# Kernel tuning notes

Measured on AMD Instinct MI355X. Metric: run time of the kernel, lower is better.

The kernel has to match this reference:

```python
import jax, jax.numpy as jnp
import numpy as np

N = 100000   # nodes
E = 1600000  # edges
D = 64       # hidden_channels (heads=1, concat)
NEG_SLOPE = 0.2


def setup_inputs() -> dict:
    key = jax.random.key(0)
    ks = jax.random.split(key, 16)
    s = (1.0 / np.sqrt(D)).astype(np.float32) if hasattr(np.sqrt(D), 'astype') else 1.0 / np.sqrt(D)
    s = 1.0 / float(np.sqrt(D))
    inp = {
        "x": jax.random.normal(ks[0], (N, D), jnp.float32),
        "edge_index": jax.random.randint(ks[1], (2, E), 0, N, dtype=jnp.int32).astype(jnp.int64),
        "edge_attr": jax.random.normal(ks[2], (E, 1), jnp.float32),
        # layer 1 params (PyG GATConv, heads=1): lin, lin_edge, att_src, att_dst, att_edge, bias
        "W1":  jax.random.normal(ks[3], (D, D), jnp.float32) * s,
        "We1": jax.random.normal(ks[4], (1, D), jnp.float32) * s,
        "as1": jax.random.normal(ks[5], (D,), jnp.float32) * s,
        "ad1": jax.random.normal(ks[6], (D,), jnp.float32) * s,
        "ae1": jax.random.normal(ks[7], (D,), jnp.float32) * s,
        "b1":  jnp.zeros((D,), jnp.float32),
        # layer 2 params
        "W2":  jax.random.normal(ks[8], (D, D), jnp.float32) * s,
        "We2": jax.random.normal(ks[9], (1, D), jnp.float32) * s,
        "as2": jax.random.normal(ks[10], (D,), jnp.float32) * s,
        "ad2": jax.random.normal(ks[11], (D,), jnp.float32) * s,
        "ae2": jax.random.normal(ks[12], (D,), jnp.float32) * s,
        "b2":  jnp.zeros((D,), jnp.float32),
    }
    return inp


def _gat_layer(x, src, dst, edge_attr, W, We, a_src, a_dst, a_edge, bias):
    """PyG GATConv, heads=1, add_self_loops=False, edge_dim=1."""
    n = x.shape[0]
    h = x @ W                      # [N, D]  transformed node features
    he = edge_attr @ We            # [E, D]  transformed edge features
    # per-node attention logits, gathered per edge
    alpha = ((h * a_src).sum(-1)[src]
             + (h * a_dst).sum(-1)[dst]
             + (he * a_edge).sum(-1))               # [E]
    alpha = jax.nn.leaky_relu(alpha, NEG_SLOPE)
    # segment softmax over incoming edges of each dst node
    m = jax.ops.segment_max(alpha, dst, num_segments=n)   # [N]
    m = jnp.where(jnp.isfinite(m), m, 0.0)
    e = jnp.exp(alpha - m[dst])                            # [E]
    denom = jax.ops.segment_sum(e, dst, num_segments=n) + 1e-16
    w = e / denom[dst]                                     # [E]
    # weighted scatter-add aggregation of source features
    out = jax.ops.segment_sum(h[src] * w[:, None], dst, num_segments=n)
    return out + bias


def reference(x, edge_index, edge_attr,
              W1, We1, as1, ad1, ae1, b1,
              W2, We2, as2, ad2, ae2, b2):
    src = edge_index[0]
    dst = edge_index[1]
    h = _gat_layer(x, src, dst, edge_attr, W1, We1, as1, ad1, ae1, b1)
    h = jax.nn.relu(h)
    out = _gat_layer(h, src, dst, edge_attr, W2, We2, as2, ad2, ae2, b2)
    return out
```

## Files before the change

kernel.cpp:

```cpp
#include <hip/hip_runtime.h>
#include <hip/hip_fp16.h>
#include <stdint.h>

#define D 64
constexpr float NEG_SLOPE = 0.2f;
#define NPB_SHIFT 9
#define NPB 512
#define PCHUNK 4096

__global__ void k_ce(const float* __restrict__ We1, const float* __restrict__ ae1,
                     const float* __restrict__ We2, const float* __restrict__ ae2,
                     float* __restrict__ ce){
  int lane = threadIdx.x;
  float p1 = We1[lane] * ae1[lane];
  float p2 = We2[lane] * ae2[lane];
  #pragma unroll
  for (int off = 32; off; off >>= 1){ p1 += __shfl_xor(p1, off); p2 += __shfl_xor(p2, off); }
  if (lane == 0){ ce[0] = p1; ce[1] = p2; }
}

__global__ __launch_bounds__(256) void k_gemm_dots(
    const float* __restrict__ X, const float* __restrict__ W,
    const float* __restrict__ a_s, const float* __restrict__ a_d,
    __half* __restrict__ H, float* __restrict__ asrc, float* __restrict__ adst, int n)
{
  __shared__ float sX[4 * 512];
  int lane = threadIdx.x & 63;
  int wv   = threadIdx.x >> 6;
  float* tile = sX + wv * 512;
  int wid  = blockIdx.x * 4 + wv;
  int nw   = gridDim.x * 4;
  float Wc[64];
  #pragma unroll
  for (int k = 0; k < 64; ++k) Wc[k] = W[k * D + lane];
  float asv = a_s[lane], adv = a_d[lane];
  int ngrp = (n + 7) >> 3;
  for (int g = wid; g < ngrp; g += nw){
    int r0 = g << 3;
    if (r0 + 8 <= n){
      const float4* Xg = (const float4*)(X + (size_t)r0 * D);
      float4 t0 = Xg[lane * 2], t1 = Xg[lane * 2 + 1];
      ((float4*)tile)[lane * 2]     = t0;
      ((float4*)tile)[lane * 2 + 1] = t1;
      __builtin_amdgcn_wave_barrier();
      float acc[8];
      #pragma unroll
      for (int j = 0; j < 8; ++j) acc[j] = 0.f;
      #pragma unroll
      for (int j = 0; j < 8; ++j){
        #pragma unroll
        for (int kb = 0; kb < 16; ++kb){
          float4 xv = ((const float4*)(tile + j * 64))[kb];
          acc[j] = fmaf(xv.x, Wc[kb * 4 + 0], acc[j]);
          acc[j] = fmaf(xv.y, Wc[kb * 4 + 1], acc[j]);
          acc[j] = fmaf(xv.z, Wc[kb * 4 + 2], acc[j]);
          acc[j] = fmaf(xv.w, Wc[kb * 4 + 3], acc[j]);
        }
      }
      #pragma unroll
      for (int j = 0; j < 8; ++j) H[(size_t)(r0 + j) * D + lane] = __float2half(acc[j]);
      #pragma unroll
      for (int j = 0; j < 8; ++j){
        float ps = acc[j] * asv, pd = acc[j] * adv;
        #pragma unroll
        for (int off = 32; off; off >>= 1){ ps += __shfl_xor(ps, off); pd += __shfl_xor(pd, off); }
        if (lane == 0){ asrc[r0 + j] = ps; adst[r0 + j] = pd; }
      }
    } else {
      for (int j = 0; r0 + j < n; ++j){
        float acc = 0.f;
        #pragma unroll
        for (int kb = 0; kb < 16; ++kb){
          float4 xv = *(const float4*)(X + (size_t)(r0 + j) * D + kb * 4);
          acc = fmaf(xv.x, Wc[kb * 4 + 0], acc);
          acc = fmaf(xv.y, Wc[kb * 4 + 1], acc);
          acc = fmaf(xv.z, Wc[kb * 4 + 2], acc);
          acc = fmaf(xv.w, Wc[kb * 4 + 3], acc);
        }
        H[(size_t)(r0 + j) * D + lane] = __float2half(acc);
        float ps = acc * asv, pd = acc * adv;
        #pragma unroll
        for (int off = 32; off; off >>= 1){ ps += __shfl_xor(ps, off); pd += __shfl_xor(pd, off); }
        if (lane == 0){ asrc[r0 + j] = ps; adst[r0 + j] = pd; }
      }
    }
  }
}


__global__ __launch_bounds__(256) void k_bhist(const int* __restrict__ dst,
    int* __restrict__ C, int nchunk, int e, int nbkt){
  __shared__ int hist[256];
  int tid = threadIdx.x, c = blockIdx.x;
  if (tid < nbkt) hist[tid] = 0;
  __syncthreads();
  int c0 = c * PCHUNK;
  #pragma unroll
  for (int k = 0; k < PCHUNK / 256; ++k){
    int i = c0 + tid + (k << 8);
    if (i < e) atomicAdd(&hist[dst[i] >> NPB_SHIFT], 1);
  }
  __syncthreads();
  if (tid < nbkt) C[tid * nchunk + c] = hist[tid];
}

__global__ __launch_bounds__(512) void k_cscan(int* __restrict__ C,
    int* __restrict__ btot, int nchunk){
  __shared__ int s[512];
  int b = blockIdx.x, tid = threadIdx.x;
  int v = (tid < nchunk) ? C[b * nchunk + tid] : 0;
  s[tid] = v; __syncthreads();
  #pragma unroll
  for (int off = 1; off < 512; off <<= 1){
    int t = (tid >= off) ? s[tid - off] : 0;
    __syncthreads();
    s[tid] += t;
    __syncthreads();
  }
  if (tid < nchunk) C[b * nchunk + tid] = s[tid] - v;
  if (tid == 511) btot[b] = s[511];
}

__global__ __launch_bounds__(256) void k_bscan(const int* __restrict__ btot,
    int* __restrict__ gbase, int nbkt){
  __shared__ int s[256];
  int tid = threadIdx.x;
  int v = (tid < nbkt) ? btot[tid] : 0;
  s[tid] = v; __syncthreads();
  #pragma unroll
  for (int off = 1; off < 256; off <<= 1){
    int t = (tid >= off) ? s[tid - off] : 0;
    __syncthreads();
    s[tid] += t;
    __syncthreads();
  }
  if (tid < nbkt) gbase[tid] = s[tid] - v;
  if (tid == 255) gbase[nbkt] = s[255];
}

__global__ __launch_bounds__(256) void k_part(const int* __restrict__ src,
    const int* __restrict__ dst, const float* __restrict__ ea,
    const int* __restrict__ gbase, const int* __restrict__ C, int nchunk,
    int2* __restrict__ staging, int e, int nbkt){
  __shared__ int base[256], cnt[256];
  int tid = threadIdx.x, c = blockIdx.x;
  if (tid < nbkt){ base[tid] = gbase[tid] + C[tid * nchunk + c]; cnt[tid] = 0; }
  __syncthreads();
  int c0 = c * PCHUNK;
  int w0[PCHUNK / 256], w1[PCHUNK / 256], bk[PCHUNK / 256];
  #pragma unroll
  for (int k = 0; k < PCHUNK / 256; ++k){
    int i = c0 + tid + (k << 8);
    bk[k] = -1;
    if (i < e){
      int d = dst[i];
      bk[k] = d >> NPB_SHIFT;
      w0[k] = src[i] | ((d & (NPB - 1)) << 17);
      w1[k] = __float_as_int(ea[i]);
    }
  }
  #pragma unroll
  for (int k = 0; k < PCHUNK / 256; ++k){
    if (bk[k] >= 0){
      int pos = base[bk[k]] + atomicAdd(&cnt[bk[k]], 1);
      staging[pos] = make_int2(w0[k], w1[k]);
    }
  }
}

__global__ __launch_bounds__(512) void k_bucket(const int* __restrict__ gbase,
    const int2* __restrict__ staging, int2* __restrict__ edges,
    int* __restrict__ rowptr, int n, int nbkt){
  __shared__ int degL[NPB], sc[NPB];
  int b = blockIdx.x, tid = threadIdx.x;
  int node0 = b << NPB_SHIFT;
  int nn = min(NPB, n - node0);
  int base = gbase[b], endj = gbase[b + 1];
  degL[tid] = 0;
  __syncthreads();
  for (int j = base + tid; j < endj; j += NPB)
    atomicAdd(&degL[staging[j].x >> 17], 1);
  __syncthreads();
  int dv = degL[tid];
  sc[tid] = dv;
  __syncthreads();
  #pragma unroll
  for (int off = 1; off < NPB; off <<= 1){
    int t = (tid >= off) ? sc[tid - off] : 0;
    __syncthreads();
    sc[tid] += t;
    __syncthreads();
  }
  int ex = sc[tid] - dv;
  if (tid < nn) rowptr[node0 + tid] = base + ex;
  if (b == nbkt - 1 && tid == 0) rowptr[n] = base + sc[NPB - 1];
  __syncthreads();
  degL[tid] = ex;
  __syncthreads();
  for (int j = base + tid; j < endj; j += NPB){
    int2 w = staging[j];
    int dloc = w.x >> 17;
    int pos = base + atomicAdd(&degL[dloc], 1);
    edges[pos] = make_int2(w.x & 0x1FFFF, w.y);
  }
}

__global__ __launch_bounds__(256) void k_node_fused(
    const int* __restrict__ rowptr, const int2* __restrict__ edges,
    const float* __restrict__ asrc, const float* __restrict__ adst,
    const float* __restrict__ ce, int ce_idx,
    const __half* __restrict__ H, const float* __restrict__ bias,
    float* __restrict__ out, int n, int relu)
{
  int lane = threadIdx.x & 63;
  int wv   = threadIdx.x >> 6;
  int vbase = (blockIdx.x * 4 + wv) * 2;
  if (vbase >= n) return;
  int h  = lane >> 5;
  int li = lane & 31;
  int v  = vbase + h;
  bool vok = v < n;
  int start = 0, end = 0;
  if (vok){ start = rowptr[v]; end = rowptr[v + 1]; }
  int deg = end - start;
  int degmax = max(deg, __shfl_xor(deg, 32));
  float cev = ce[ce_idx];

  if (degmax <= 32){
    int my_s = 0; float my_e = 0.f;
    if (li < deg){
      int2 pr = edges[start + li];
      my_s = pr.x;
      float a = asrc[pr.x] + adst[v] + __int_as_float(pr.y) * cev;
      a = a > 0.f ? a : NEG_SLOPE * a;
      my_e = __expf(a);
    }
    int sub = li >> 4;
    int fq  = li & 15;
    const uint2* H2 = (const uint2*)H;
    int eb = h * 32 + sub;
    int sP[8]; float wP[8]; uint2 uP[8];
    #pragma unroll
    for (int p = 0; p < 8; ++p) sP[p] = __shfl(my_s, eb + 2 * p);
    #pragma unroll
    for (int p = 0; p < 8; ++p) uP[p] = H2[(size_t)sP[p] * 16 + fq];
    float ss = my_e;
    #pragma unroll
    for (int off = 16; off; off >>= 1) ss += __shfl_xor(ss, off);
    float inv = 1.f / (ss + 1e-16f);
    #pragma unroll
    for (int p = 0; p < 8; ++p) wP[p] = __shfl(my_e, eb + 2 * p);
    float a0 = 0.f, a1 = 0.f, a2 = 0.f, a3 = 0.f;
    #pragma unroll
    for (int p = 0; p < 8; ++p){
      __half2 q0 = *(const __half2*)&uP[p].x;
      __half2 q1 = *(const __half2*)&uP[p].y;
      float2 f0 = __half22float2(q0);
      float2 f1 = __half22float2(q1);
      a0 = fmaf(f0.x, wP[p], a0);
      a1 = fmaf(f0.y, wP[p], a1);
      a2 = fmaf(f1.x, wP[p], a2);
      a3 = fmaf(f1.y, wP[p], a3);
    }
    if (degmax > 16){
      #pragma unroll
      for (int p = 0; p < 8; ++p) sP[p] = __shfl(my_s, eb + 16 + 2 * p);
      #pragma unroll
      for (int p = 0; p < 8; ++p) uP[p] = H2[(size_t)sP[p] * 16 + fq];
      #pragma unroll
      for (int p = 0; p < 8; ++p) wP[p] = __shfl(my_e, eb + 16 + 2 * p);
      #pragma unroll
      for (int p = 0; p < 8; ++p){
        __half2 q0 = *(const __half2*)&uP[p].x;
        __half2 q1 = *(const __half2*)&uP[p].y;
        float2 f0 = __half22float2(q0);
        float2 f1 = __half22float2(q1);
        a0 = fmaf(f0.x, wP[p], a0);
        a1 = fmaf(f0.y, wP[p], a1);
        a2 = fmaf(f1.x, wP[p], a2);
        a3 = fmaf(f1.y, wP[p], a3);
      }
    }
    a0 += __shfl_xor(a0, 16);
    a1 += __shfl_xor(a1, 16);
    a2 += __shfl_xor(a2, 16);
    a3 += __shfl_xor(a3, 16);
    if (vok && li < 16){
      float4 bv = ((const float4*)bias)[li];
      float4 r;
      r.x = a0 * inv + bv.x;
      r.y = a1 * inv + bv.y;
      r.z = a2 * inv + bv.z;
      r.w = a3 * inv + bv.w;
      if (relu){
        r.x = fmaxf(r.x, 0.f); r.y = fmaxf(r.y, 0.f);
        r.z = fmaxf(r.z, 0.f); r.w = fmaxf(r.w, 0.f);
      }
      ((float4*)(out + (size_t)v * D))[li] = r;
    }
  } else {
    for (int t = 0; t < 2; ++t){
      int vv = vbase + t;
      if (vv >= n) break;
      int st = rowptr[vv], en = rowptr[vv + 1];
      int dg = en - st;
      if (dg == 0){
        float bv = bias[lane];
        float r = relu ? fmaxf(bv, 0.f) : bv;
        out[(size_t)vv * D + lane] = r;
        continue;
      }
      float adv = adst[vv];
      if (dg <= 64){
        int my_s = 0; float my_e = 0.f;
        if (lane < dg){
          int2 pr = edges[st + lane];
          my_s = pr.x;
          float a = asrc[pr.x] + adv + __int_as_float(pr.y) * cev;
          a = a > 0.f ? a : NEG_SLOPE * a;
          my_e = __expf(a);
        }
        int hf = lane >> 5;
        int fp = lane & 31;
        const __half2* Hp = (const __half2*)H;
        float ss = my_e;
        #pragma unroll
        for (int off = 32; off; off >>= 1) ss += __shfl_xor(ss, off);
        float inv = 1.f / (ss + 1e-16f);
        float accx = 0.f, accy = 0.f;
        for (int k = 0; k < dg; k += 16){
          #pragma unroll
          for (int p = 0; p < 8; ++p){
            int ix = k + 2 * p + hf; ix = ix > 63 ? 63 : ix;
            int s0 = __shfl(my_s, ix);
            float w0 = __shfl(my_e, ix);
            float2 hv = __half22float2(Hp[(size_t)s0 * 32 + fp]);
            accx = fmaf(hv.x, w0, accx);
            accy = fmaf(hv.y, w0, accy);
          }
        }
        accx += __shfl_xor(accx, 32);
        accy += __shfl_xor(accy, 32);
        if (lane < 32){
          float2 bv2 = ((const float2*)bias)[fp];
          float2 r;
          r.x = accx * inv + bv2.x;
          r.y = accy * inv + bv2.y;
          if (relu){ r.x = fmaxf(r.x, 0.f); r.y = fmaxf(r.y, 0.f); }
          ((float2*)(out + (size_t)vv * D))[fp] = r;
        }
      } else {
        float bv = bias[lane];
        float c0 = 0.f, c1 = 0.f, c2 = 0.f, c3 = 0.f;
        float ss = 0.f;
        for (int j0 = st; j0 < en; j0 += 64){
          int j = j0 + lane;
          int my_s = 0; float my_e = 0.f;
          if (j < en){
            int2 pr = edges[j];
            float a = asrc[pr.x] + adv + __int_as_float(pr.y) * cev;
            a = a > 0.f ? a : NEG_SLOPE * a;
            my_e = __expf(a);
            my_s = pr.x;
          }
          ss += my_e;
          int cnt = min(64, en - j0);
          int k = 0;
          for (; k + 4 <= cnt; k += 4){
            int s0 = __shfl(my_s, k+0), s1 = __shfl(my_s, k+1);
            int s2 = __shfl(my_s, k+2), s3 = __shfl(my_s, k+3);
            float w0 = __shfl(my_e, k+0), w1 = __shfl(my_e, k+1);
            float w2 = __shfl(my_e, k+2), w3 = __shfl(my_e, k+3);
            float h0 = __half2float(H[(size_t)s0 * D + lane]);
            float h1 = __half2float(H[(size_t)s1 * D + lane]);
            float h2 = __half2float(H[(size_t)s2 * D + lane]);
            float h3 = __half2float(H[(size_t)s3 * D + lane]);
            c0 = fmaf(h0, w0, c0); c1 = fmaf(h1, w1, c1);
            c2 = fmaf(h2, w2, c2); c3 = fmaf(h3, w3, c3);
          }
          for (; k < cnt; ++k){
            int s0 = __shfl(my_s, k);
            float w0 = __shfl(my_e, k);
            c0 = fmaf(__half2float(H[(size_t)s0 * D + lane]), w0, c0);
          }
        }
        #pragma unroll
        for (int off = 32; off; off >>= 1) ss += __shfl_xor(ss, off);
        float inv = 1.f / (ss + 1e-16f);
        float acc = (c0 + c1) + (c2 + c3);
        float r = acc * inv + bv;
        if (relu) r = fmaxf(r, 0.f);
        out[(size_t)vv * D + lane] = r;
      }
    }
  }
}

extern "C" void kernel_launch(void* const* d_in, const int* in_sizes, int n_in,
                              void* d_out, int out_size, void* d_ws, size_t ws_size,
                              hipStream_t stream)
{
  const float* x    = (const float*)d_in[0];
  const int*   ei   = (const int*)d_in[1];
  const float* ea   = (const float*)d_in[2];
  const float* W1   = (const float*)d_in[3];
  const float* We1  = (const float*)d_in[4];
  const float* as1  = (const float*)d_in[5];
  const float* ad1  = (const float*)d_in[6];
  const float* ae1  = (const float*)d_in[7];
  const float* b1   = (const float*)d_in[8];
  const float* W2   = (const float*)d_in[9];
  const float* We2  = (const float*)d_in[10];
  const float* as2  = (const float*)d_in[11];
  const float* ad2  = (const float*)d_in[12];
  const float* ae2  = (const float*)d_in[13];
  const float* b2   = (const float*)d_in[14];
  float* out = (float*)d_out;

  int n = in_sizes[0] / D;
  int e = in_sizes[1] / 2;
  const int* srcp = ei;
  const int* dstp = ei + e;

  int nbkt   = (n + NPB - 1) / NPB;
  int nchunk = (e + PCHUNK - 1) / PCHUNK;

  char* p = (char*)d_ws;
  __half* buf_h  = (__half*)p; p += (size_t)n * D * 2;
  float* buf_x2  = (float*)p;  p += (size_t)n * D * 4;
  float* asrc    = (float*)p;  p += (size_t)n * 4;
  float* adst    = (float*)p;  p += (size_t)n * 4;
  int*   rowptr  = (int*)p;    p += (size_t)(n + 16) * 4;
  int*   gbase   = (int*)p;    p += (size_t)(nbkt + 4) * 4;
  int*   btot    = (int*)p;    p += (size_t)(nbkt + 4) * 4;
  int*   C       = (int*)p;    p += (size_t)nbkt * nchunk * 4;
  float* ce      = (float*)p;  p += 64;
  int2*  edges   = (int2*)p;   p += (size_t)e * 8;
  int2*  staging = (int2*)buf_x2;

  int pairs = (n + 1) / 2;
  int gR = (pairs + 3) / 4;
  int gG = ((n + 7) / 8 + 3) / 4;

  k_ce<<<1, 64, 0, stream>>>(We1, ae1, We2, ae2, ce);
  k_bhist<<<nchunk, 256, 0, stream>>>(dstp, C, nchunk, e, nbkt);
  k_cscan<<<nbkt, 512, 0, stream>>>(C, btot, nchunk);
  k_bscan<<<1, 256, 0, stream>>>(btot, gbase, nbkt);
  k_part<<<nchunk, 256, 0, stream>>>(srcp, dstp, ea, gbase, C, nchunk, staging, e, nbkt);
  k_bucket<<<nbkt, NPB, 0, stream>>>(gbase, staging, edges, rowptr, n, nbkt);

  k_gemm_dots<<<gG, 256, 0, stream>>>(x, W1, as1, ad1, buf_h, asrc, adst, n);
  k_node_fused<<<gR, 256, 0, stream>>>(rowptr, edges, asrc, adst, ce, 0, buf_h, b1, buf_x2, n, 1);

  k_gemm_dots<<<gG, 256, 0, stream>>>(buf_x2, W2, as2, ad2, buf_h, asrc, adst, n);
  k_node_fused<<<gR, 256, 0, stream>>>(rowptr, edges, asrc, adst, ce, 1, buf_h, b2, out, n, 0);
}
```

Baseline: 281.5 us.

## Replace scan-based edge partition with fixed-capacity buckets and atomic offsets

```diff
diff --git a/kernel.cpp b/kernel.cpp
--- a/kernel.cpp
+++ b/kernel.cpp
@@ -7,16 +7,92 @@
 #define NPB_SHIFT 9
 #define NPB 512
 #define PCHUNK 4096
-
-__global__ void k_ce(const float* __restrict__ We1, const float* __restrict__ ae1,
-                     const float* __restrict__ We2, const float* __restrict__ ae2,
-                     float* __restrict__ ce){
-  int lane = threadIdx.x;
-  float p1 = We1[lane] * ae1[lane];
-  float p2 = We2[lane] * ae2[lane];
+#define BCAP 16384
+
+__global__ __launch_bounds__(256) void k_init(int* __restrict__ gcnt, int nbkt,
+    const float* __restrict__ We1, const float* __restrict__ ae1,
+    const float* __restrict__ We2, const float* __restrict__ ae2,
+    float* __restrict__ ce){
+  int tid = threadIdx.x;
+  if (tid < nbkt) gcnt[tid] = 0;
+  if (tid < 64){
+    float p1 = We1[tid] * ae1[tid];
+    float p2 = We2[tid] * ae2[tid];
+    #pragma unroll
+    for (int off = 32; off; off >>= 1){ p1 += __shfl_xor(p1, off); p2 += __shfl_xor(p2, off); }
+    if (tid == 0){ ce[0] = p1; ce[1] = p2; }
+  }
+}
+
+__global__ __launch_bounds__(512) void k_part2(const int* __restrict__ src,
+    const int* __restrict__ dst, const float* __restrict__ ea,
+    int* __restrict__ gcnt, int2* __restrict__ staging, int e, int nbkt){
+  __shared__ int hist[256], base[256], cnt[256];
+  int tid = threadIdx.x, c = blockIdx.x;
+  if (tid < nbkt){ hist[tid] = 0; cnt[tid] = 0; }
+  __syncthreads();
+  int c0 = c * PCHUNK;
+  int w0[PCHUNK / 512], w1[PCHUNK / 512], bk[PCHUNK / 512];
   #pragma unroll
-  for (int off = 32; off; off >>= 1){ p1 += __shfl_xor(p1, off); p2 += __shfl_xor(p2, off); }
-  if (lane == 0){ ce[0] = p1; ce[1] = p2; }
+  for (int k = 0; k < PCHUNK / 512; ++k){
+    int i = c0 + tid + (k << 9);
+    bk[k] = -1;
+    if (i < e){
+      int d = dst[i];
+      bk[k] = d >> NPB_SHIFT;
+      w0[k] = src[i] | ((d & (NPB - 1)) << 17);
+      w1[k] = __float_as_int(ea[i]);
+      atomicAdd(&hist[bk[k]], 1);
+    }
+  }
+  __syncthreads();
+  if (tid < nbkt && hist[tid] > 0)
+    base[tid] = tid * BCAP + atomicAdd(&gcnt[tid], hist[tid]);
+  __syncthreads();
+  #pragma unroll
+  for (int k = 0; k < PCHUNK / 512; ++k){
+    if (bk[k] >= 0){
+      int pos = base[bk[k]] + atomicAdd(&cnt[bk[k]], 1);
+      staging[pos] = make_int2(w0[k], w1[k]);
+    }
+  }
+}
+
+__global__ __launch_bounds__(512) void k_bucket(const int* __restrict__ gcnt,
+    const int2* __restrict__ staging, int2* __restrict__ edges,
+    int2* __restrict__ rowptr2, int n, int nbkt){
+  __shared__ int degL[NPB], sc[NPB];
+  int b = blockIdx.x, tid = threadIdx.x;
+  int node0 = b << NPB_SHIFT;
+  int nn = min(NPB, n - node0);
+  int base = b * BCAP;
+  int endj = base + gcnt[b];
+  degL[tid] = 0;
+  __syncthreads();
+  for (int j = base + tid; j < endj; j += NPB)
+    atomicAdd(&degL[staging[j].x >> 17], 1);
+  __syncthreads();
+  int dv = degL[tid];
+  sc[tid] = dv;
+  __syncthreads();
+  #pragma unroll
+  for (int off = 1; off < NPB; off <<= 1){
+    int t = (tid >= off) ? sc[tid - off] : 0;
+    __syncthreads();
+    sc[tid] += t;
+    __syncthreads();
+  }
+  int ex = sc[tid] - dv;
+  if (tid < nn) rowptr2[node0 + tid] = make_int2(base + ex, dv);
+  __syncthreads();
+  degL[tid] = ex;
+  __syncthreads();
+  for (int j = base + tid; j < endj; j += NPB){
+    int2 w = staging[j];
+    int dloc = w.x >> 17;
+    int pos = base + atomicAdd(&degL[dloc], 1);
+    edges[pos] = make_int2(w.x & 0x1FFFF, w.y);
+  }
 }
 
 __global__ __launch_bounds__(256) void k_gemm_dots(
@@ -87,126 +163,8 @@
   }
 }
 
-
-__global__ __launch_bounds__(256) void k_bhist(const int* __restrict__ dst,
-    int* __restrict__ C, int nchunk, int e, int nbkt){
-  __shared__ int hist[256];
-  int tid = threadIdx.x, c = blockIdx.x;
-  if (tid < nbkt) hist[tid] = 0;
-  __syncthreads();
-  int c0 = c * PCHUNK;
-  #pragma unroll
-  for (int k = 0; k < PCHUNK / 256; ++k){
-    int i = c0 + tid + (k << 8);
-    if (i < e) atomicAdd(&hist[dst[i] >> NPB_SHIFT], 1);
-  }
-  __syncthreads();
-  if (tid < nbkt) C[tid * nchunk + c] = hist[tid];
-}
-
-__global__ __launch_bounds__(512) void k_cscan(int* __restrict__ C,
-    int* __restrict__ btot, int nchunk){
-  __shared__ int s[512];
-  int b = blockIdx.x, tid = threadIdx.x;
-  int v = (tid < nchunk) ? C[b * nchunk + tid] : 0;
-  s[tid] = v; __syncthreads();
-  #pragma unroll
-  for (int off = 1; off < 512; off <<= 1){
-    int t = (tid >= off) ? s[tid - off] : 0;
-    __syncthreads();
-    s[tid] += t;
-    __syncthreads();
-  }
-  if (tid < nchunk) C[b * nchunk + tid] = s[tid] - v;
-  if (tid == 511) btot[b] = s[511];
-}
-
-__global__ __launch_bounds__(256) void k_bscan(const int* __restrict__ btot,
-    int* __restrict__ gbase, int nbkt){
-  __shared__ int s[256];
-  int tid = threadIdx.x;
-  int v = (tid < nbkt) ? btot[tid] : 0;
-  s[tid] = v; __syncthreads();
-  #pragma unroll
-  for (int off = 1; off < 256; off <<= 1){
-    int t = (tid >= off) ? s[tid - off] : 0;
-    __syncthreads();
-    s[tid] += t;
-    __syncthreads();
-  }
-  if (tid < nbkt) gbase[tid] = s[tid] - v;
-  if (tid == 255) gbase[nbkt] = s[255];
-}
-
-__global__ __launch_bounds__(256) void k_part(const int* __restrict__ src,
-    const int* __restrict__ dst, const float* __restrict__ ea,
-    const int* __restrict__ gbase, const int* __restrict__ C, int nchunk,
-    int2* __restrict__ staging, int e, int nbkt){
-  __shared__ int base[256], cnt[256];
-  int tid = threadIdx.x, c = blockIdx.x;
-  if (tid < nbkt){ base[tid] = gbase[tid] + C[tid * nchunk + c]; cnt[tid] = 0; }
-  __syncthreads();
-  int c0 = c * PCHUNK;
-  int w0[PCHUNK / 256], w1[PCHUNK / 256], bk[PCHUNK / 256];
-  #pragma unroll
-  for (int k = 0; k < PCHUNK / 256; ++k){
-    int i = c0 + tid + (k << 8);
-    bk[k] = -1;
-    if (i < e){
-      int d = dst[i];
-      bk[k] = d >> NPB_SHIFT;
-      w0[k] = src[i] | ((d & (NPB - 1)) << 17);
-      w1[k] = __float_as_int(ea[i]);
-    }
-  }
-  #pragma unroll
-  for (int k = 0; k < PCHUNK / 256; ++k){
-    if (bk[k] >= 0){
-      int pos = base[bk[k]] + atomicAdd(&cnt[bk[k]], 1);
-      staging[pos] = make_int2(w0[k], w1[k]);
-    }
-  }
-}
-
-__global__ __launch_bounds__(512) void k_bucket(const int* __restrict__ gbase,
-    const int2* __restrict__ staging, int2* __restrict__ edges,
-    int* __restrict__ rowptr, int n, int nbkt){
-  __shared__ int degL[NPB], sc[NPB];
-  int b = blockIdx.x, tid = threadIdx.x;
-  int node0 = b << NPB_SHIFT;
-  int nn = min(NPB, n - node0);
-  int base = gbase[b], endj = gbase[b + 1];
-  degL[tid] = 0;
-  __syncthreads();
-  for (int j = base + tid; j < endj; j += NPB)
-    atomicAdd(&degL[staging[j].x >> 17], 1);
-  __syncthreads();
-  int dv = degL[tid];
-  sc[tid] = dv;
-  __syncthreads();
-  #pragma unroll
-  for (int off = 1; off < NPB; off <<= 1){
-    int t = (tid >= off) ? sc[tid - off] : 0;
-    __syncthreads();
-    sc[tid] += t;
-    __syncthreads();
-  }
-  int ex = sc[tid] - dv;
-  if (tid < nn) rowptr[node0 + tid] = base + ex;
-  if (b == nbkt - 1 && tid == 0) rowptr[n] = base + sc[NPB - 1];
-  __syncthreads();
-  degL[tid] = ex;
-  __syncthreads();
-  for (int j = base + tid; j < endj; j += NPB){
-    int2 w = staging[j];
-    int dloc = w.x >> 17;
-    int pos = base + atomicAdd(&degL[dloc], 1);
-    edges[pos] = make_int2(w.x & 0x1FFFF, w.y);
-  }
-}
-
 __global__ __launch_bounds__(256) void k_node_fused(
-    const int* __restrict__ rowptr, const int2* __restrict__ edges,
+    const int2* __restrict__ rowptr2, const int2* __restrict__ edges,
     const float* __restrict__ asrc, const float* __restrict__ adst,
     const float* __restrict__ ce, int ce_idx,
     const __half* __restrict__ H, const float* __restrict__ bias,
@@ -220,9 +178,8 @@
   int li = lane & 31;
   int v  = vbase + h;
   bool vok = v < n;
-  int start = 0, end = 0;
-  if (vok){ start = rowptr[v]; end = rowptr[v + 1]; }
-  int deg = end - start;
+  int start = 0, deg = 0;
+  if (vok){ int2 rp = rowptr2[v]; start = rp.x; deg = rp.y; }
   int degmax = max(deg, __shfl_xor(deg, 32));
   float cev = ce[ce_idx];
 
@@ -302,8 +259,9 @@
     for (int t = 0; t < 2; ++t){
       int vv = vbase + t;
       if (vv >= n) break;
-      int st = rowptr[vv], en = rowptr[vv + 1];
-      int dg = en - st;
+      int2 rp = rowptr2[vv];
+      int st = rp.x, dg = rp.y;
+      int en = st + dg;
       if (dg == 0){
         float bv = bias[lane];
         float r = relu ? fmaxf(bv, 0.f) : bv;
@@ -430,28 +388,25 @@
   float* buf_x2  = (float*)p;  p += (size_t)n * D * 4;
   float* asrc    = (float*)p;  p += (size_t)n * 4;
   float* adst    = (float*)p;  p += (size_t)n * 4;
-  int*   rowptr  = (int*)p;    p += (size_t)(n + 16) * 4;
-  int*   gbase   = (int*)p;    p += (size_t)(nbkt + 4) * 4;
-  int*   btot    = (int*)p;    p += (size_t)(nbkt + 4) * 4;
-  int*   C       = (int*)p;    p += (size_t)nbkt * nchunk * 4;
+  int2*  rowptr2 = (int2*)p;   p += (size_t)(n + 16) * 8;
+  int*   gcnt    = (int*)p;    p += 1024;
   float* ce      = (float*)p;  p += 64;
-  int2*  edges   = (int2*)p;   p += (size_t)e * 8;
-  int2*  staging = (int2*)buf_x2;
+  int2*  staging = (int2*)p;   p += (size_t)nbkt * BCAP * 8;
+  int2*  edges   = (int2*)p;   p += (size_t)nbkt * BCAP * 8;
 
   int pairs = (n + 1) / 2;
   int gR = (pairs + 3) / 4;
-  int gG = ((n + 7) / 8 + 3) / 4;
-
-  k_ce<<<1, 64, 0, stream>>>(We1, ae1, We2, ae2, ce);
-  k_bhist<<<nchunk, 256, 0, stream>>>(dstp, C, nchunk, e, nbkt);
-  k_cscan<<<nbkt, 512, 0, stream>>>(C, btot, nchunk);
-  k_bscan<<<1, 256, 0, stream>>>(btot, gbase, nbkt);
-  k_part<<<nchunk, 256, 0, stream>>>(srcp, dstp, ea, gbase, C, nchunk, staging, e, nbkt);
-  k_bucket<<<nbkt, NPB, 0, stream>>>(gbase, staging, edges, rowptr, n, nbkt);
+  int ngrp = (n + 7) / 8;
+  int gG = (ngrp + 3) / 4; if (gG > 1024) gG = 1024;
+
+  k_init<<<1, 256, 0, stream>>>(gcnt, nbkt, We1, ae1, We2, ae2, ce);
+  k_part2<<<nchunk, 512, 0, stream>>>(srcp, dstp, ea, gcnt, staging, e, nbkt);
+  k_bucket<<<nbkt, NPB, 0, stream>>>(gcnt, staging, edges, rowptr2, n, nbkt);
 
   k_gemm_dots<<<gG, 256, 0, stream>>>(x, W1, as1, ad1, buf_h, asrc, adst, n);
-  k_node_fused<<<gR, 256, 0, stream>>>(rowptr, edges, asrc, adst, ce, 0, buf_h, b1, buf_x2, n, 1);
-
+  k_node_fused<<<gR, 256, 0, stream>>>(rowptr2, edges, asrc, adst, ce, 0,
+      buf_h, b1, buf_x2, n, 1);
   k_gemm_dots<<<gG, 256, 0, stream>>>(buf_x2, W2, as2, ad2, buf_h, asrc, adst, n);
-  k_node_fused<<<gR, 256, 0, stream>>>(rowptr, edges, asrc, adst, ce, 1, buf_h, b2, out, n, 0);
-}
+  k_node_fused<<<gR, 256, 0, stream>>>(rowptr2, edges, asrc, adst, ce, 1,
+      buf_h, b2, out, n, 0);
+}
```

Result: faster. 274.0 us (median of 2 runs) (-2.6%).
